# Kernel tuning notes

Measured on AMD Instinct MI355X. Metric: run time of the kernel, lower is better.

## Reference

```python
import jax, jax.numpy as jnp
import numpy as np

BN_EPS = 1e-5
NUM_HEADS = 4
PROJ = 512

def _bn(x, gamma, beta, mean, var):
    # eval-mode BatchNorm1d over last dim
    return (x - mean) * jax.lax.rsqrt(var + BN_EPS) * gamma + beta

def setup_inputs() -> dict:
    key = jax.random.key(0)
    ks = jax.random.split(key, 12)
    B, Tq, Tk, D = 32, 256, 1024, 512
    inp = {
        "s": jax.random.normal(ks[0], (B, Tq, D), jnp.float32),
        "h": jax.random.normal(ks[1], (B, Tk, D), jnp.float32),
        "phi_gamma": jnp.ones((D,), jnp.float32),
        "phi_beta": jnp.zeros((D,), jnp.float32),
        "phi_mean": 0.1 * jax.random.normal(ks[2], (D,), jnp.float32),
        "phi_var": jax.random.uniform(ks[3], (D,), jnp.float32, 0.5, 1.5),
        "W_phi": 0.02 * jax.random.normal(ks[4], (PROJ * NUM_HEADS, D), jnp.float32),
        "psi_gamma": jnp.ones((D,), jnp.float32),
        "psi_beta": jnp.zeros((D,), jnp.float32),
        "psi_mean": 0.1 * jax.random.normal(ks[5], (D,), jnp.float32),
        "psi_var": jax.random.uniform(ks[6], (D,), jnp.float32, 0.5, 1.5),
        "W_psi": 0.02 * jax.random.normal(ks[7], (PROJ, D), jnp.float32),
        "red_gamma": jnp.ones((D * NUM_HEADS,), jnp.float32),
        "red_beta": jnp.zeros((D * NUM_HEADS,), jnp.float32),
        "red_mean": 0.1 * jax.random.normal(ks[8], (D * NUM_HEADS,), jnp.float32),
        "red_var": jax.random.uniform(ks[9], (D * NUM_HEADS,), jnp.float32, 0.5, 1.5),
        "W_red": 0.02 * jax.random.normal(ks[10], (D, D * NUM_HEADS), jnp.float32),
    }
    return inp

def reference(s, h, phi_gamma, phi_beta, phi_mean, phi_var, W_phi,
              psi_gamma, psi_beta, psi_mean, psi_var, W_psi,
              red_gamma, red_beta, red_mean, red_var, W_red):
    B, Tq, _ = s.shape
    # phi: BN + Linear on decoder states -> (B, Tq, H*PROJ)
    ms = _bn(s, phi_gamma, phi_beta, phi_mean, phi_var) @ W_phi.T
    # psi: BN + Linear on encoder states -> (B, Tk, PROJ)
    mh = _bn(h, psi_gamma, psi_beta, psi_mean, psi_var) @ W_psi.T
    # split heads along last dim of ms (matches torch.split order)
    ms4 = ms.reshape(B, Tq, NUM_HEADS, PROJ)
    # unscaled dot-product scores per head: (H, B, Tq, Tk)
    e = jnp.einsum("bqhd,bkd->hbqk", ms4, mh)
    a = jax.nn.softmax(e, axis=-1)
    # context uses the ORIGINAL h (not mh): (B, Tq, H, D) -> concat heads
    ctx = jnp.einsum("hbqk,bkv->bqhv", a, h).reshape(B, Tq, -1)
    # reduce: BN + Linear -> (B, Tq, D)
    c = _bn(ctx, red_gamma, red_beta, red_mean, red_var) @ W_red.T
    return (a, c)
```

## Files before the change

kernel.cpp:

```cpp
#include <hip/hip_runtime.h>

typedef short s8v __attribute__((ext_vector_type(8)));
typedef float f4v __attribute__((ext_vector_type(4)));

static constexpr int Bc = 32, Tq = 256, Tkc = 1024, Dc = 512, Hc = 4;
static constexpr float BN_EPS = 1e-5f;

__device__ inline ushort f2bf(float x) {
    union { float f; unsigned int u; } v; v.f = x;
    unsigned int r = v.u + 0x7fff + ((v.u >> 16) & 1);
    return (ushort)(r >> 16);
}

__global__ __launch_bounds__(256) void fold_bn(
    const float* __restrict__ W, const float* __restrict__ gamma,
    const float* __restrict__ beta, const float* __restrict__ mean,
    const float* __restrict__ var, ushort* __restrict__ Wp,
    float* __restrict__ bias, int K)
{
    int n = blockIdx.x;
    int tid = threadIdx.x;
    float acc = 0.f;
    for (int k = tid; k < K; k += 256) {
        float sc = gamma[k] * rsqrtf(var[k] + BN_EPS);
        float sh = beta[k] - mean[k] * sc;
        float w = W[(long)n * K + k];
        Wp[(long)n * K + k] = f2bf(w * sc);
        acc = fmaf(w, sh, acc);
    }
    __shared__ float red[256];
    red[tid] = acc;
    __syncthreads();
    for (int s = 128; s > 0; s >>= 1) {
        if (tid < s) red[tid] += red[tid + s];
        __syncthreads();
    }
    if (tid == 0) bias[n] = red[0];
}

__global__ __launch_bounds__(256) void f32_to_bf16(
    const float* __restrict__ x, ushort* __restrict__ y)
{
    long i = ((long)blockIdx.x * 256 + threadIdx.x) * 4;
    float4 v = *(const float4*)&x[i];
    ushort4 o = { f2bf(v.x), f2bf(v.y), f2bf(v.z), f2bf(v.w) };
    *(ushort4*)&y[i] = o;
}

__global__ __launch_bounds__(256) void conv_h(
    const float* __restrict__ h, ushort* __restrict__ h_bf,
    ushort* __restrict__ hT)
{
    __shared__ float tl[64][65];
    int b = blockIdx.z, k0 = blockIdx.y * 64, d0 = blockIdx.x * 64;
    int t = threadIdx.x, r = t >> 4, c = (t & 15) * 4;
    const float* hb = h + ((long)b * Tkc + k0) * Dc + d0;
    ushort* sb = h_bf + ((long)b * Tkc + k0) * Dc + d0;
    #pragma unroll
    for (int i = 0; i < 4; i++) {
        int rr = r + i * 16;
        float4 v = *(const float4*)&hb[(long)rr * Dc + c];
        tl[rr][c + 0] = v.x; tl[rr][c + 1] = v.y;
        tl[rr][c + 2] = v.z; tl[rr][c + 3] = v.w;
        ushort4 sv = { f2bf(v.x), f2bf(v.y), f2bf(v.z), f2bf(v.w) };
        *(ushort4*)&sb[(long)rr * Dc + c] = sv;
    }
    __syncthreads();
    ushort* o = hT + ((long)b * Dc + d0) * Tkc + k0;
    #pragma unroll
    for (int i = 0; i < 4; i++) {
        int dr = r + i * 16;
        ushort4 ov = { f2bf(tl[c + 0][dr]), f2bf(tl[c + 1][dr]),
                       f2bf(tl[c + 2][dr]), f2bf(tl[c + 3][dr]) };
        *(ushort4*)&o[(long)dr * Tkc + c] = ov;
    }
}

__global__ __launch_bounds__(256) void init_c(
    float* __restrict__ C, const float* __restrict__ bias)
{
    long i = (long)blockIdx.x * 256 + threadIdx.x;
    int n4 = (int)(i & 127);
    float4 b = ((const float4*)bias)[n4];
    ((float4*)C)[i] = b;
}

typedef __attribute__((address_space(1))) void gvoid;
typedef __attribute__((address_space(3))) void lvoid;

#define GLOAD(gp, lp) __builtin_amdgcn_global_load_lds((gvoid*)(gp), (lvoid*)(lp), 16, 0, 0)
#define BAR() asm volatile("s_barrier" ::: "memory")
#define WAITV0() asm volatile("s_waitcnt vmcnt(0)" ::: "memory")

__global__ __launch_bounds__(256, 4) void gemm_mfma(
    const ushort* __restrict__ A, const ushort* __restrict__ B,
    float* __restrict__ Cf, ushort* __restrict__ Cb,
    const float* __restrict__ bias, int atom,
    int K, int lda, int ldb, int ldc,
    long sAh, long sAb, long sBh, long sBb, long sCh, long sCb,
    int nB, int nxs, int zbits)
{
    int bx = blockIdx.x;
    int z = bx & ((1 << zbits) - 1);
    int j2 = bx >> zbits;
    int gx = j2 & ((1 << nxs) - 1);
    int gy = j2 >> nxs;

    int hh = z / nB, bb = z - hh * nB;
    A += hh * sAh + bb * sAb;
    B += hh * sBh + bb * sBb;
    long coff = hh * sCh + bb * sCb;

    __shared__ ushort Als[128 * 64];
    __shared__ ushort Bls[128 * 64];

    int tid = threadIdx.x;
    int l = tid & 63, w = tid >> 6;
    int m0 = gy * 128, n0 = gx * 128;

    const ushort* gA[4]; const ushort* gB[4];
    ushort* lA[4]; ushort* lB[4];
    #pragma unroll
    for (int j = 0; j < 4; j++) {
        int L = (w * 4 + j) * 64 + l;
        int m = L >> 3, c = L & 7;
        int kof = (c ^ ((m >> 1) & 7)) * 8;
        gA[j] = A + (long)(m0 + m) * lda + kof;
        gB[j] = B + (long)(n0 + m) * ldb + kof;
        lA[j] = &Als[(w * 4 + j) * 512];
        lB[j] = &Bls[(w * 4 + j) * 512];
    }

    int wm = (w >> 1) * 64, wn = (w & 1) * 64;
    int fr = l & 15, kc = l >> 4;

    int aidx[2][4], bidx[2][4];
    #pragma unroll
    for (int kk = 0; kk < 2; kk++)
        #pragma unroll
        for (int t = 0; t < 4; t++) {
            int ra = wm + t * 16 + fr;
            aidx[kk][t] = (ra * 8 + ((kk * 4 + kc) ^ ((ra >> 1) & 7))) * 8;
            int rb = wn + t * 16 + fr;
            bidx[kk][t] = (rb * 8 + ((kk * 4 + kc) ^ ((rb >> 1) & 7))) * 8;
        }

    f4v acc[4][4] = {};

    for (int k0 = 0; k0 < K; k0 += 64) {
        #pragma unroll
        for (int j = 0; j < 4; j++) {
            GLOAD(gA[j] + k0, lA[j]);
            GLOAD(gB[j] + k0, lB[j]);
        }
        __syncthreads();
        #pragma unroll
        for (int kk = 0; kk < 2; kk++) {
            s8v af[4], bfv[4];
            #pragma unroll
            for (int t = 0; t < 4; t++) af[t]  = *(const s8v*)&Als[aidx[kk][t]];
            #pragma unroll
            for (int t = 0; t < 4; t++) bfv[t] = *(const s8v*)&Bls[bidx[kk][t]];
            #pragma unroll
            for (int i = 0; i < 4; i++)
                #pragma unroll
                for (int jj = 0; jj < 4; jj++)
                    acc[i][jj] = __builtin_amdgcn_mfma_f32_16x16x32_bf16(
                        af[i], bfv[jj], acc[i][jj], 0, 0, 0);
        }
        __syncthreads();
    }

    #pragma unroll
    for (int i = 0; i < 4; i++) {
        #pragma unroll
        for (int jj = 0; jj < 4; jj++) {
            int n = n0 + wn + jj * 16 + fr;
            float bv = bias ? bias[n] : 0.f;
            #pragma unroll
            for (int r = 0; r < 4; r++) {
                int m = m0 + wm + i * 16 + kc * 4 + r;
                float v = acc[i][jj][r] + bv;
                long off = coff + (long)m * ldc + n;
                if (atom)    atomicAdd(&Cf[off], v);
                else if (Cb) Cb[off] = f2bf(v);
                else         Cf[off] = v;
            }
        }
    }
}

#define FBUF 34816

#define FSTG(t, bufb) do { \
    if (w < 4) GLOAD(gAs + (t) * 32, &lds[(bufb) + w * 512]); \
    _Pragma("unroll") \
    for (int j = 0; j < 8; j++) \
        GLOAD(gBs + j * 8192 + (t) * 32, &lds[(bufb) + 2048 + (w * 8 + j) * 512]); \
} while (0)

#define FCOMP(bufb) do { \
    s8v aF[4]; \
    _Pragma("unroll") \
    for (int mi = 0; mi < 4; mi++) \
        aF[mi] = *(const s8v*)&lds[(bufb) + mi * 512 + l * 8]; \
    _Pragma("unroll") \
    for (int j = 0; j < 8; j++) { \
        s8v bF = *(const s8v*)&lds[(bufb) + 2048 + (w * 8 + j) * 512 + l * 8]; \
        _Pragma("unroll") \
        for (int mi = 0; mi < 4; mi++) \
            acc[mi][j] = __builtin_amdgcn_mfma_f32_16x16x32_bf16( \
                aF[mi], bF, acc[mi][j], 0, 0, 0); \
    } \
} while (0)

__global__ __launch_bounds__(512, 2) void fused_esm(
    const ushort* __restrict__ ms, const ushort* __restrict__ mh,
    float* __restrict__ outA, ushort* __restrict__ aB, int lognb)
{
    __shared__ ushort lds[69632];

    int bx = blockIdx.x;
    int bbl = bx & ((1 << lognb) - 1);
    int hm = bx >> lognb;
    int hh = hm >> 2, mt = hm & 3;
    int nb = 1 << lognb;

    int tid = threadIdx.x;
    int w = tid >> 6, l = tid & 63;

    const ushort* gAs = ms + ((long)(bbl * 256 + mt * 64 + (w & 3) * 16 + (l & 15))) * 2048
                           + hh * 512 + ((l >> 4) * 8);
    const ushort* gBs = mh + ((long)(bbl * 1024 + w * 128 + (l & 15))) * 512
                           + ((l >> 4) * 8);

    f4v acc[4][8] = {};

    FSTG(0, 0); WAITV0(); BAR();
    #pragma unroll 1
    for (int t2 = 0; t2 < 7; ++t2) {
        FSTG(2 * t2 + 1, FBUF); FCOMP(0);    WAITV0(); BAR();
        FSTG(2 * t2 + 2, 0);    FCOMP(FBUF); WAITV0(); BAR();
    }
    FSTG(15, FBUF); FCOMP(0); WAITV0(); BAR();
    FCOMP(FBUF);

    __syncthreads();
    float* red = (float*)lds;
    int g4 = l >> 4;

    float mxv[4][4];
    #pragma unroll
    for (int mi = 0; mi < 4; mi++)
        #pragma unroll
        for (int r = 0; r < 4; r++) {
            float m_ = acc[mi][0][r];
            #pragma unroll
            for (int j = 1; j < 8; j++) m_ = fmaxf(m_, acc[mi][j][r]);
            m_ = fmaxf(m_, __shfl_xor(m_, 1, 64));
            m_ = fmaxf(m_, __shfl_xor(m_, 2, 64));
            m_ = fmaxf(m_, __shfl_xor(m_, 4, 64));
            m_ = fmaxf(m_, __shfl_xor(m_, 8, 64));
            mxv[mi][r] = m_;
        }
    if ((l & 15) == 0) {
        #pragma unroll
        for (int mi = 0; mi < 4; mi++)
            #pragma unroll
            for (int r = 0; r < 4; r++)
                red[w * 64 + mi * 16 + g4 * 4 + r] = mxv[mi][r];
    }
    __syncthreads();
    if (tid < 64) {
        float m_ = red[tid];
        #pragma unroll
        for (int ww = 1; ww < 8; ww++) m_ = fmaxf(m_, red[ww * 64 + tid]);
        red[512 + tid] = m_;
    }
    __syncthreads();
    #pragma unroll
    for (int mi = 0; mi < 4; mi++) {
        float4 f = *(const float4*)&red[512 + mi * 16 + g4 * 4];
        mxv[mi][0] = f.x; mxv[mi][1] = f.y; mxv[mi][2] = f.z; mxv[mi][3] = f.w;
    }

    float smv[4][4];
    #pragma unroll
    for (int mi = 0; mi < 4; mi++)
        #pragma unroll
        for (int r = 0; r < 4; r++) {
            float s_ = 0.f;
            #pragma unroll
            for (int j = 0; j < 8; j++) {
                float e = __expf(acc[mi][j][r] - mxv[mi][r]);
                acc[mi][j][r] = e;
                s_ += e;
            }
            s_ += __shfl_xor(s_, 1, 64);
            s_ += __shfl_xor(s_, 2, 64);
            s_ += __shfl_xor(s_, 4, 64);
            s_ += __shfl_xor(s_, 8, 64);
            smv[mi][r] = s_;
        }
    if ((l & 15) == 0) {
        #pragma unroll
        for (int mi = 0; mi < 4; mi++)
            #pragma unroll
            for (int r = 0; r < 4; r++)
                red[w * 64 + mi * 16 + g4 * 4 + r] = smv[mi][r];
    }
    __syncthreads();
    if (tid < 64) {
        float s_ = red[tid];
        #pragma unroll
        for (int ww = 1; ww < 8; ww++) s_ += red[ww * 64 + tid];
        red[512 + tid] = 1.f / s_;
    }
    __syncthreads();
    #pragma unroll
    for (int mi = 0; mi < 4; mi++) {
        float4 f = *(const float4*)&red[512 + mi * 16 + g4 * 4];
        smv[mi][0] = f.x; smv[mi][1] = f.y; smv[mi][2] = f.z; smv[mi][3] = f.w;
    }

    float* oA = outA + ((long)(hh * 32 + bbl) * 256 + mt * 64) * 1024;
    ushort* oB = aB + ((long)(hh * nb + bbl) * 256 + mt * 64) * 1024;
    #pragma unroll
    for (int mi = 0; mi < 4; mi++)
        #pragma unroll
        for (int j = 0; j < 8; j++)
            #pragma unroll
            for (int r = 0; r < 4; r++) {
                int rr = mi * 16 + g4 * 4 + r;
                int cc = w * 128 + j * 16 + (l & 15);
                float p = acc[mi][j][r] * smv[mi][r];
                oA[(long)rr * 1024 + cc] = p;
                oB[(long)rr * 1024 + cc] = f2bf(p);
            }
}

extern "C" void kernel_launch(void* const* d_in, const int* in_sizes, int n_in,
                              void* d_out, int out_size, void* d_ws, size_t ws_size,
                              hipStream_t stream)
{
    const float* s     = (const float*)d_in[0];
    const float* h     = (const float*)d_in[1];
    const float* phi_g = (const float*)d_in[2];
    const float* phi_b = (const float*)d_in[3];
    const float* phi_m = (const float*)d_in[4];
    const float* phi_v = (const float*)d_in[5];
    const float* W_phi = (const float*)d_in[6];
    const float* psi_g = (const float*)d_in[7];
    const float* psi_b = (const float*)d_in[8];
    const float* psi_m = (const float*)d_in[9];
    const float* psi_v = (const float*)d_in[10];
    const float* W_psi = (const float*)d_in[11];
    const float* red_g = (const float*)d_in[12];
    const float* red_b = (const float*)d_in[13];
    const float* red_m = (const float*)d_in[14];
    const float* red_v = (const float*)d_in[15];
    const float* W_red = (const float*)d_in[16];

    float* out_a = (float*)d_out;
    float* out_c = out_a + (long)Hc * Bc * Tq * Tkc;

    char* p = (char*)d_ws;
    ushort* Wphi_b = (ushort*)p;  p += (long)2048 * 512 * 2;
    ushort* Wpsi_b = (ushort*)p;  p += (long)512 * 512 * 2;
    ushort* Wred_b = (ushort*)p;  p += (long)512 * 2048 * 2;
    float* bias_phi = (float*)p;  p += 2048 * 4;
    float* bias_psi = (float*)p;  p += 512 * 4;
    float* bias_red = (float*)p;  p += 512 * 4;
    ushort* s_bf  = (ushort*)p;   p += (long)8192 * 512 * 2;
    ushort* h_bf  = (ushort*)p;   p += (long)32768 * 512 * 2;
    ushort* hT_bf = (ushort*)p;   p += (long)32768 * 512 * 2;
    ushort* ms_bf = (ushort*)p;   p += (long)8192 * 2048 * 2;
    ushort* mh_bf = (ushort*)p;   p += (long)32768 * 512 * 2;

    long avail = (long)ws_size - (p - (char*)d_ws);
    int S, lognb;
    ushort *aReg, *ctxReg;
    if (avail >= (long)64 * 1024 * 1024) {
        S = 1; lognb = 5;
        aReg = (ushort*)p;
        ctxReg = s_bf;
    } else if (avail >= (long)16 * 1024 * 1024) {
        S = 2; lognb = 4;
        aReg = s_bf;
        ctxReg = (ushort*)p;
    } else {
        S = 4; lognb = 3;
        aReg = s_bf;
        ctxReg = s_bf + (long)8 * 1024 * 1024;
    }
    int nb = 32 / S;

    fold_bn<<<2048, 256, 0, stream>>>(W_phi, phi_g, phi_b, phi_m, phi_v, Wphi_b, bias_phi, 512);
    fold_bn<<<512,  256, 0, stream>>>(W_psi, psi_g, psi_b, psi_m, psi_v, Wpsi_b, bias_psi, 512);
    fold_bn<<<512,  256, 0, stream>>>(W_red, red_g, red_b, red_m, red_v, Wred_b, bias_red, 2048);

    f32_to_bf16<<<4096, 256, 0, stream>>>(s, s_bf);
    conv_h<<<dim3(8, 16, 32), 256, 0, stream>>>(h, h_bf, hT_bf);
    init_c<<<4096, 256, 0, stream>>>(out_c, bias_red);

    gemm_mfma<<<16 * 64, 256, 0, stream>>>(
        s_bf, Wphi_b, nullptr, ms_bf, bias_phi, 0,
        512, 512, 512, 2048, 0, 0, 0, 0, 0, 0, 1, 4, 0);

    gemm_mfma<<<4 * 256, 256, 0, stream>>>(
        h_bf, Wpsi_b, nullptr, mh_bf, bias_psi, 0,
        512, 512, 512, 512, 0, 0, 0, 0, 0, 0, 1, 2, 0);

    for (int q = 0; q < S; q++) {
        fused_esm<<<16 * nb, 512, 0, stream>>>(
            ms_bf + (long)q * nb * 256 * 2048,
            mh_bf + (long)q * nb * 1024 * 512,
            out_a + (long)q * nb * 256 * 1024,
            aReg, lognb);

        gemm_mfma<<<8 * 4 * nb, 256, 0, stream>>>(
            aReg, hT_bf + (long)q * nb * 512 * 1024, nullptr, ctxReg, nullptr, 0,
            1024, 1024, 1024, 2048,
             (long)nb * 256 * 1024,  (long)256 * 1024,
             0,  (long)512 * 1024,
             512,  (long)256 * 2048,
            nb, 2, lognb + 2);

        gemm_mfma<<<(2 * nb) * 4 * 4, 256, 0, stream>>>(
            ctxReg, Wred_b, out_c + (long)q * nb * 256 * 512, nullptr, nullptr, 1,
            512, 2048, 2048, 512,
             512,  0,
             512,  0,
             0,  0,
            1, 2, 2);
    }
}
```

Before: 552.4 us.

## Single-buffer score GEMM LDS and stage softmax output through LDS for vector stores

Drops the double-buffered LDS staging in the fused score/softmax kernel in favour of a single buffer with load-wait-compute-barrier per K step, roughly halving shared memory per block. The softmax epilogue now writes each wave's normalized tile into an LDS slab and reads it back so that fp32 and bf16 attention outputs are stored as contiguous float4/ushort4 row segments instead of scattered scalar stores. Lower LDS use may allow more resident blocks, but loads no longer overlap MFMA compute within a block.

```diff
diff --git a/kernel.cpp b/kernel.cpp
--- a/kernel.cpp
+++ b/kernel.cpp
@@ -190,23 +190,21 @@
     }
 }
 
-#define FBUF 34816
-
-#define FSTG(t, bufb) do { \
-    if (w < 4) GLOAD(gAs + (t) * 32, &lds[(bufb) + w * 512]); \
+#define FSTG(t) do { \
+    if (w < 4) GLOAD(gAs + (t) * 32, &lds[w * 512]); \
     _Pragma("unroll") \
     for (int j = 0; j < 8; j++) \
-        GLOAD(gBs + j * 8192 + (t) * 32, &lds[(bufb) + 2048 + (w * 8 + j) * 512]); \
+        GLOAD(gBs + j * 8192 + (t) * 32, &lds[2048 + (w * 8 + j) * 512]); \
 } while (0)
 
-#define FCOMP(bufb) do { \
+#define FCOMP() do { \
     s8v aF[4]; \
     _Pragma("unroll") \
     for (int mi = 0; mi < 4; mi++) \
-        aF[mi] = *(const s8v*)&lds[(bufb) + mi * 512 + l * 8]; \
+        aF[mi] = *(const s8v*)&lds[mi * 512 + l * 8]; \
     _Pragma("unroll") \
     for (int j = 0; j < 8; j++) { \
-        s8v bF = *(const s8v*)&lds[(bufb) + 2048 + (w * 8 + j) * 512 + l * 8]; \
+        s8v bF = *(const s8v*)&lds[2048 + (w * 8 + j) * 512 + l * 8]; \
         _Pragma("unroll") \
         for (int mi = 0; mi < 4; mi++) \
             acc[mi][j] = __builtin_amdgcn_mfma_f32_16x16x32_bf16( \
@@ -218,7 +216,7 @@
     const ushort* __restrict__ ms, const ushort* __restrict__ mh,
     float* __restrict__ outA, ushort* __restrict__ aB, int lognb)
 {
-    __shared__ ushort lds[69632];
+    __shared__ ushort lds[36864];
 
     int bx = blockIdx.x;
     int bbl = bx & ((1 << lognb) - 1);
@@ -236,14 +234,13 @@
 
     f4v acc[4][8] = {};
 
-    FSTG(0, 0); WAITV0(); BAR();
     #pragma unroll 1
-    for (int t2 = 0; t2 < 7; ++t2) {
-        FSTG(2 * t2 + 1, FBUF); FCOMP(0);    WAITV0(); BAR();
-        FSTG(2 * t2 + 2, 0);    FCOMP(FBUF); WAITV0(); BAR();
-    }
-    FSTG(15, FBUF); FCOMP(0); WAITV0(); BAR();
-    FCOMP(FBUF);
+    for (int t = 0; t < 16; ++t) {
+        FSTG(t);
+        WAITV0(); BAR();
+        FCOMP();
+        BAR();
+    }
 
     __syncthreads();
     float* red = (float*)lds;
@@ -322,21 +319,33 @@
         float4 f = *(const float4*)&red[512 + mi * 16 + g4 * 4];
         smv[mi][0] = f.x; smv[mi][1] = f.y; smv[mi][2] = f.z; smv[mi][3] = f.w;
     }
-
+    __syncthreads();
+
+    float* slab = (float*)lds + w * 2304;
     float* oA = outA + ((long)(hh * 32 + bbl) * 256 + mt * 64) * 1024;
     ushort* oB = aB + ((long)(hh * nb + bbl) * 256 + mt * 64) * 1024;
-    #pragma unroll
-    for (int mi = 0; mi < 4; mi++)
-        #pragma unroll
-        for (int j = 0; j < 8; j++)
-            #pragma unroll
-            for (int r = 0; r < 4; r++) {
-                int rr = mi * 16 + g4 * 4 + r;
-                int cc = w * 128 + j * 16 + (l & 15);
-                float p = acc[mi][j][r] * smv[mi][r];
-                oA[(long)rr * 1024 + cc] = p;
-                oB[(long)rr * 1024 + cc] = f2bf(p);
-            }
+    int c = l & 15;
+    #pragma unroll 1
+    for (int jp = 0; jp < 4; jp++) {
+        #pragma unroll
+        for (int mi = 0; mi < 4; mi++)
+            #pragma unroll
+            for (int jd = 0; jd < 2; jd++)
+                #pragma unroll
+                for (int r = 0; r < 4; r++)
+                    slab[(mi * 16 + g4 * 4 + r) * 36 + jd * 16 + c] =
+                        acc[mi][jp * 2 + jd][r] * smv[mi][r];
+        #pragma unroll
+        for (int i = 0; i < 8; i++) {
+            int idx = i * 64 + l;
+            int rr = idx >> 3, q = idx & 7;
+            float4 v4 = *(const float4*)&slab[rr * 36 + q * 4];
+            int col = w * 128 + jp * 32 + q * 4;
+            *(float4*)&oA[(long)rr * 1024 + col] = v4;
+            ushort4 o4 = { f2bf(v4.x), f2bf(v4.y), f2bf(v4.z), f2bf(v4.w) };
+            *(ushort4*)&oB[(long)rr * 1024 + col] = o4;
+        }
+    }
 }
 
 extern "C" void kernel_launch(void* const* d_in, const int* in_sizes, int n_in,
```

Result: slower. 707.6 us (+28.1%).
